# Performance work log

Hardware: AMD Instinct MI355X
Metric: run time of the kernel (lower is better)

Reference implementation:

```python
import jax, jax.numpy as jnp
import numpy as np

H = 128      # hidden_dim
ED = 16      # edge_dim
N = 50000    # n_nodes
E = 500000   # n_edges
B = 1
EPS = 1e-5


def setup_inputs() -> dict:
    key = jax.random.key(0)
    ks = jax.random.split(key, 16)
    s = 0.02
    inp = {
        "h": jax.random.normal(ks[0], (B, N, H), jnp.float32),
        "edge_attr": jax.random.normal(ks[1], (B, E, ED), jnp.float32),
        "edge_index": jax.random.randint(ks[2], (E, 2), 0, N, jnp.int32),
        # src_proj
        "src_W": jax.random.normal(ks[3], (H, H), jnp.float32) * s,
        "src_b": jnp.zeros((H,), jnp.float32),
        # edge_net: Linear(2H+ED -> H), GELU, Linear(H -> 2H)
        "e1_W": jax.random.normal(ks[4], (2 * H + ED, H), jnp.float32) * s,
        "e1_b": jnp.zeros((H,), jnp.float32),
        "e2_W": jax.random.normal(ks[5], (H, 2 * H), jnp.float32) * s,
        "e2_b": jnp.zeros((2 * H,), jnp.float32),
        # self_proj / agg_proj
        "self_W": jax.random.normal(ks[6], (H, H), jnp.float32) * s,
        "self_b": jnp.zeros((H,), jnp.float32),
        "agg_W": jax.random.normal(ks[7], (H, H), jnp.float32) * s,
        "agg_b": jnp.zeros((H,), jnp.float32),
        # LayerNorm
        "ln_g": jnp.ones((H,), jnp.float32),
        "ln_b": jnp.zeros((H,), jnp.float32),
    }
    return inp


def reference(h, edge_attr, edge_index, src_W, src_b, e1_W, e1_b, e2_W, e2_b,
              self_W, self_b, agg_W, agg_b, ln_g, ln_b):
    src = edge_index[:, 0]
    dst = edge_index[:, 1]

    h_src = h[:, src, :]                      # [B, E, H]
    h_dst = h[:, dst, :]                      # [B, E, H]
    edge_input = jnp.concatenate([h_src, h_dst, edge_attr], axis=-1)  # [B, E, 2H+ED]

    hid = jax.nn.gelu(edge_input @ e1_W + e1_b, approximate=False)    # [B, E, H]
    edge_ctx = hid @ e2_W + e2_b                                      # [B, E, 2H]
    gate, shift = jnp.split(edge_ctx, 2, axis=-1)
    msg = jax.nn.sigmoid(gate) * (h_src @ src_W + src_b) + shift      # [B, E, H]

    # scatter-add over destination nodes
    agg = jnp.zeros_like(h).at[:, dst, :].add(msg)                    # [B, N, H]
    indeg = jnp.maximum(jnp.zeros((N,), h.dtype).at[dst].add(1.0), 1.0)
    agg = agg / indeg[None, :, None]

    update = (h @ self_W + self_b) + (agg @ agg_W + agg_b)
    x = h + jax.nn.gelu(update, approximate=False)

    mu = jnp.mean(x, axis=-1, keepdims=True)
    var = jnp.var(x, axis=-1, keepdims=True)
    return (x - mu) / jnp.sqrt(var + EPS) * ln_g + ln_b
```

## Files before the change

### kernel.cpp

```cpp
#include <hip/hip_runtime.h>
#include <hip/hip_bf16.h>
#include <math.h>

#define NN 50000
#define NE 500000
#define LN_EPS 1e-5f

typedef __attribute__((ext_vector_type(8))) short short8;
typedef __attribute__((ext_vector_type(4))) float f32x4;

__device__ __forceinline__ unsigned short f2bf(float f) {
    unsigned int u = __float_as_uint(f);
    u = (u + 0x7FFFu + ((u >> 16) & 1u)) >> 16;
    return (unsigned short)u;
}
__device__ __forceinline__ float bf2f(unsigned short b) {
    return __uint_as_float(((unsigned int)b) << 16);
}
__device__ __forceinline__ float sigm_f(float x) {
    return 1.0f / (1.0f + __expf(-x));
}
__device__ __forceinline__ float gelu_fast(float x) {
    return x * sigm_f(1.5957691f * fmaf(0.044715f * x * x, x, x));
}

__global__ __launch_bounds__(256) void pack_kernel(
    const float* __restrict__ src_W, const float* __restrict__ e1_W,
    const float* __restrict__ e2_W,
    const float* __restrict__ self_W, const float* __restrict__ agg_W,
    unsigned short* __restrict__ p1, unsigned short* __restrict__ p2,
    unsigned short* __restrict__ p3, float2* __restrict__ p4)
{
    const int fid = blockIdx.x * 256 + threadIdx.x;
    if (fid < 6144) {
        const int g = fid / 384, t = fid % 384;
        const int nn = g >> 2, kk = g & 3;
        const int w = t / 64, lane = t & 63, lo = lane & 15, hi = lane >> 4;
        const int c = w * 64 + nn * 16 + lo;
        short8 v;
        #pragma unroll
        for (int j = 0; j < 8; ++j) {
            const int k = kk * 32 + hi * 8 + j;
            float wv;
            if (c < 128)      wv = src_W[k * 128 + c];
            else if (c < 256) wv = e1_W[k * 128 + (c - 128)];
            else              wv = e1_W[(128 + k) * 128 + (c - 256)];
            v[j] = (short)f2bf(wv);
        }
        *(short8*)(p1 + (g * 384 + t) * 8) = v;
    } else if (fid < 10240) {
        const int f = fid - 6144;
        const int g = f / 256, t = f % 256;
        const int nn = g >> 3, kk = g & 7;
        const int w = t / 64, lane = t & 63, lo = lane & 15, hi = lane >> 4;
        const int c = w * 32 + nn * 16 + lo;
        short8 v;
        #pragma unroll
        for (int j = 0; j < 8; ++j) {
            const int k = kk * 32 + hi * 8 + j;
            const float wv = (k < 128) ? self_W[k * 128 + c] : agg_W[(k - 128) * 128 + c];
            v[j] = (short)f2bf(wv);
        }
        *(short8*)(p2 + (g * 256 + t) * 8) = v;
    } else if (fid < 14336) {
        const int f = fid - 10240;
        const int g = f / 256, t = f % 256;
        const int nn = g >> 2, kk = g & 3;
        const int w = t / 64, lane = t & 63, lo = lane & 15, hi = lane >> 4;
        const int nbase = (nn < 2) ? (w * 32 + nn * 16) : (128 + w * 32 + (nn - 2) * 16);
        const int n = nbase + lo;
        short8 v;
        #pragma unroll
        for (int j = 0; j < 8; ++j) {
            const int k = kk * 32 + hi * 8 + j;
            v[j] = (short)f2bf(e2_W[k * 256 + n]);
        }
        *(short8*)(p3 + (g * 256 + t) * 8) = v;
    } else if (fid < 15360) {
        const int f = fid - 14336;
        const int lane = f / 16, k = f % 16;
        p4[lane * 16 + k] = make_float2(e1_W[(256 + k) * 128 + 2 * lane],
                                        e1_W[(256 + k) * 128 + 2 * lane + 1]);
    }
}

__global__ __launch_bounds__(384) void node_pre_kernel(
    const float* __restrict__ h,
    const float* __restrict__ src_b, const float* __restrict__ e1_b,
    const unsigned short* __restrict__ p1,
    unsigned short* __restrict__ hswb,
    unsigned short* __restrict__ a1b,
    unsigned short* __restrict__ b1b)
{
    const int tid = threadIdx.x;
    const int lane = tid & 63;
    const int w = tid >> 6;
    const int lo = lane & 15, hi = lane >> 4;
    const int m0 = blockIdx.x * 64;

    short8 bf[4][4];
    #pragma unroll
    for (int nn = 0; nn < 4; ++nn)
        #pragma unroll
        for (int kk = 0; kk < 4; ++kk)
            bf[kk][nn] = *(const short8*)(p1 + ((nn * 4 + kk) * 384 + tid) * 8);

    f32x4 acc[4][4];
    #pragma unroll
    for (int mm = 0; mm < 4; ++mm)
        #pragma unroll
        for (int nn = 0; nn < 4; ++nn)
            acc[mm][nn] = (f32x4){0.f, 0.f, 0.f, 0.f};

    #pragma unroll
    for (int mm = 0; mm < 4; ++mm) {
        int row = m0 + mm * 16 + lo;
        if (row >= NN) row = NN - 1;
        short8 af[4];
        #pragma unroll
        for (int kk = 0; kk < 4; ++kk) {
            const float* pp = h + row * 128 + kk * 32 + hi * 8;
            const float4 q0 = *(const float4*)pp;
            const float4 q1 = *(const float4*)(pp + 4);
            short8 v;
            v[0] = (short)f2bf(q0.x); v[1] = (short)f2bf(q0.y);
            v[2] = (short)f2bf(q0.z); v[3] = (short)f2bf(q0.w);
            v[4] = (short)f2bf(q1.x); v[5] = (short)f2bf(q1.y);
            v[6] = (short)f2bf(q1.z); v[7] = (short)f2bf(q1.w);
            af[kk] = v;
        }
        #pragma unroll
        for (int nn = 0; nn < 4; ++nn)
            #pragma unroll
            for (int kk = 0; kk < 4; ++kk)
                acc[mm][nn] = __builtin_amdgcn_mfma_f32_16x16x32_bf16(
                    af[kk], bf[kk][nn], acc[mm][nn], 0, 0, 0);
    }

    #pragma unroll
    for (int mm = 0; mm < 4; ++mm) {
        #pragma unroll
        for (int nn = 0; nn < 4; ++nn) {
            const int c = w * 64 + nn * 16 + lo;
            #pragma unroll
            for (int r = 0; r < 4; ++r) {
                const int row = m0 + mm * 16 + hi * 4 + r;
                if (row < NN) {
                    const float v = acc[mm][nn][r];
                    if (c < 128)      hswb[row * 128 + c]       = f2bf(v + src_b[c]);
                    else if (c < 256) a1b [row * 128 + (c-128)] = f2bf(v + e1_b[c-128]);
                    else              b1b [row * 128 + (c-256)] = f2bf(v);
                }
            }
        }
    }
}

__global__ __launch_bounds__(256) void hist_kernel(
    const int* __restrict__ edge_index, int* __restrict__ deg)
{
    const int e = blockIdx.x * 256 + threadIdx.x;
    if (e < NE) atomicAdd(&deg[edge_index[2 * e + 1]], 1);
}

__global__ __launch_bounds__(1024) void scan_kernel(
    const int* __restrict__ deg, int* __restrict__ cursor)
{
    __shared__ int sums[1024];
    const int t = threadIdx.x;
    const int chunk = (NN + 1023) / 1024;
    const int i0 = t * chunk;
    int s = 0;
    for (int i = 0; i < chunk; ++i) {
        const int idx = i0 + i;
        if (idx < NN) s += deg[idx];
    }
    sums[t] = s;
    __syncthreads();
    for (int off = 1; off < 1024; off <<= 1) {
        const int v = (t >= off) ? sums[t - off] : 0;
        __syncthreads();
        sums[t] += v;
        __syncthreads();
    }
    int run = (t > 0) ? sums[t - 1] : 0;
    for (int i = 0; i < chunk; ++i) {
        const int idx = i0 + i;
        if (idx < NN) {
            cursor[idx] = run;
            run += deg[idx];
        }
    }
}

__global__ __launch_bounds__(256) void scatter_kernel(
    const int* __restrict__ edge_index, const float* __restrict__ edge_attr,
    int* __restrict__ cursor,
    int* __restrict__ s_sorted, int* __restrict__ d_sorted,
    unsigned short* __restrict__ ea_sorted)
{
    const int e = blockIdx.x * 256 + threadIdx.x;
    if (e < NE) {
        const int s = edge_index[2 * e];
        const int d = edge_index[2 * e + 1];
        const int pos = atomicAdd(&cursor[d], 1);
        s_sorted[pos] = s;
        d_sorted[pos] = d;
        const float4 q0 = *(const float4*)(edge_attr + e * 16);
        const float4 q1 = *(const float4*)(edge_attr + e * 16 + 4);
        const float4 q2 = *(const float4*)(edge_attr + e * 16 + 8);
        const float4 q3 = *(const float4*)(edge_attr + e * 16 + 12);
        short8 vl, vh;
        vl[0] = (short)f2bf(q0.x); vl[1] = (short)f2bf(q0.y);
        vl[2] = (short)f2bf(q0.z); vl[3] = (short)f2bf(q0.w);
        vl[4] = (short)f2bf(q1.x); vl[5] = (short)f2bf(q1.y);
        vl[6] = (short)f2bf(q1.z); vl[7] = (short)f2bf(q1.w);
        vh[0] = (short)f2bf(q2.x); vh[1] = (short)f2bf(q2.y);
        vh[2] = (short)f2bf(q2.z); vh[3] = (short)f2bf(q2.w);
        vh[4] = (short)f2bf(q3.x); vh[5] = (short)f2bf(q3.y);
        vh[6] = (short)f2bf(q3.z); vh[7] = (short)f2bf(q3.w);
        *(short8*)(ea_sorted + (size_t)pos * 16)     = vl;
        *(short8*)(ea_sorted + (size_t)pos * 16 + 8) = vh;
    }
}

__global__ __launch_bounds__(256, 2) void edge_kernel(
    const unsigned short* __restrict__ ea_sorted,
    const int* __restrict__ s_sorted, const int* __restrict__ d_sorted,
    const unsigned short* __restrict__ p3, const float2* __restrict__ p4,
    const float* __restrict__ e2_b,
    const unsigned short* __restrict__ hswb,
    const unsigned short* __restrict__ a1b, const unsigned short* __restrict__ b1b,
    float* __restrict__ agg, int nblocks)
{
    __shared__ unsigned int hid32[64 * 64];
    __shared__ unsigned int hswt[64 * 64];
    __shared__ int s_lds[2][64];
    __shared__ int d_lds[2][64];

    const int tid = threadIdx.x;
    const int lane = tid & 63;
    const int w = __builtin_amdgcn_readfirstlane(tid >> 6);
    const int lo = lane & 15, hi = lane >> 4;

    float2 e1c[16];
    #pragma unroll
    for (int k = 0; k < 16; ++k) e1c[k] = p4[lane * 16 + k];

    short8 bf[4][4];
    #pragma unroll
    for (int nn = 0; nn < 4; ++nn)
        #pragma unroll
        for (int kk = 0; kk < 4; ++kk)
            bf[kk][nn] = *(const short8*)(p3 + ((nn * 4 + kk) * 256 + tid) * 8);
    float bg[2], bs[2];
    #pragma unroll
    for (int nn = 0; nn < 2; ++nn) {
        bg[nn] = e2_b[w * 32 + nn * 16 + lo];
        bs[nn] = e2_b[128 + w * 32 + nn * 16 + lo];
    }

    const int chunk = (nblocks + (int)gridDim.x - 1) / (int)gridDim.x;
    const int t0 = blockIdx.x * chunk;
    const int t1 = min(t0 + chunk, nblocks);
    if (t0 >= t1) return;

    if (tid < 64) {
        const int ti = t0 * 64 + tid;
        s_lds[0][tid] = (ti < NE) ? s_sorted[ti] : 0;
        d_lds[0][tid] = (ti < NE) ? d_sorted[ti] : -1;
    }
    __syncthreads();

    int p = 0;
    for (int t = t0; t < t1; ++t) {
        const long base = (long)t * 64;

        #pragma unroll
        for (int half = 0; half < 2; ++half) {
            unsigned int av[8], bv[8], hv[8];
            #pragma unroll
            for (int u = 0; u < 8; ++u) {
                const int er = w * 16 + half * 8 + u;
                const int s = s_lds[p][er];
                int d = d_lds[p][er]; if (d < 0) d = 0;
                av[u] = *(const unsigned int*)(a1b  + (size_t)s * 128 + 2 * lane);
                bv[u] = *(const unsigned int*)(b1b  + (size_t)d * 128 + 2 * lane);
                hv[u] = *(const unsigned int*)(hswb + (size_t)s * 128 + 2 * lane);
            }
            #pragma unroll
            for (int u = 0; u < 8; ++u) {
                const int er = w * 16 + half * 8 + u;
                hswt[er * 64 + (lane ^ (((er >> 2) & 3) << 3))] = hv[u];
                float tA = bf2f((unsigned short)(av[u] & 0xFFFFu))
                         + bf2f((unsigned short)(bv[u] & 0xFFFFu));
                float tB = bf2f((unsigned short)(av[u] >> 16))
                         + bf2f((unsigned short)(bv[u] >> 16));
                const short8 eaL = *(const short8*)(ea_sorted + (base + er) * 16);
                const short8 eaH = *(const short8*)(ea_sorted + (base + er) * 16 + 8);
                #pragma unroll
                for (int k = 0; k < 8; ++k) {
                    const float e = bf2f((unsigned short)eaL[k]);
                    tA = fmaf(e, e1c[k].x, tA);
                    tB = fmaf(e, e1c[k].y, tB);
                }
                #pragma unroll
                for (int k = 0; k < 8; ++k) {
                    const float e = bf2f((unsigned short)eaH[k]);
                    tA = fmaf(e, e1c[8 + k].x, tA);
                    tB = fmaf(e, e1c[8 + k].y, tB);
                }
                tA = gelu_fast(tA);
                tB = gelu_fast(tB);
                const unsigned int hp = (unsigned int)f2bf(tA) | ((unsigned int)f2bf(tB) << 16);
                const int ch = (lane >> 2) ^ (er & 7);
                hid32[er * 64 + ch * 4 + (lane & 3)] = hp;
            }
        }

        int sN = 0, dN = -1;
        const bool more = (t + 1 < t1);
        if (more && tid < 64) {
            const int ti = (t + 1) * 64 + tid;
            if (ti < NE) { sN = s_sorted[ti]; dN = d_sorted[ti]; }
        }
        __syncthreads();

        f32x4 acc[4][4];
        #pragma unroll
        for (int mm = 0; mm < 4; ++mm)
            #pragma unroll
            for (int nn = 0; nn < 4; ++nn)
                acc[mm][nn] = (f32x4){0.f, 0.f, 0.f, 0.f};

        #pragma unroll
        for (int mm = 0; mm < 4; ++mm) {
            const int row = mm * 16 + lo;
            short8 af[4];
            #pragma unroll
            for (int kk = 0; kk < 4; ++kk) {
                const int sb = ((kk * 4 + hi) ^ (row & 7)) << 4;
                af[kk] = *(const short8*)((const char*)hid32 + row * 256 + sb);
            }
            #pragma unroll
            for (int nn = 0; nn < 4; ++nn)
                #pragma unroll
                for (int kk = 0; kk < 4; ++kk)
                    acc[mm][nn] = __builtin_amdgcn_mfma_f32_16x16x32_bf16(
                        af[kk], bf[kk][nn], acc[mm][nn], 0, 0, 0);
        }

        #pragma unroll
        for (int mm = 0; mm < 4; ++mm) {
            #pragma unroll
            for (int nn = 0; nn < 2; ++nn) {
                const int c = w * 32 + nn * 16 + lo;
                int pd = -1;
                float pend = 0.f;
                #pragma unroll
                for (int r = 0; r < 4; ++r) {
                    const int er = mm * 16 + hi * 4 + r;
                    const int d = d_lds[p][er];
                    if (d >= 0) {
                        const float g  = acc[mm][nn][r]     + bg[nn];
                        const float sh = acc[mm][nn + 2][r] + bs[nn];
                        const unsigned int hw =
                            hswt[er * 64 + ((c >> 1) ^ (((er >> 2) & 3) << 3))];
                        const float hval =
                            bf2f((unsigned short)((c & 1) ? (hw >> 16) : (hw & 0xFFFFu)));
                        const float msg = sigm_f(g) * hval + sh;
                        if (d != pd) {
                            if (pd >= 0) unsafeAtomicAdd(&agg[(size_t)pd * 128 + c], pend);
                            pd = d; pend = 0.f;
                        }
                        pend += msg;
                    }
                }
                if (pd >= 0) unsafeAtomicAdd(&agg[(size_t)pd * 128 + c], pend);
            }
        }

        if (more && tid < 64) {
            s_lds[p ^ 1][tid] = sN;
            d_lds[p ^ 1][tid] = dN;
        }
        __syncthreads();
        p ^= 1;
    }
}

__global__ __launch_bounds__(256) void node_post_kernel(
    const float* __restrict__ h,
    const float* __restrict__ self_b, const float* __restrict__ agg_b,
    const float* __restrict__ ln_g, const float* __restrict__ ln_b,
    const float* __restrict__ agg, const int* __restrict__ deg,
    const unsigned short* __restrict__ p2,
    float* __restrict__ out)
{
    __shared__ float x_lds[64 * 129];
    const int tid = threadIdx.x;
    const int lane = tid & 63;
    const int w = tid >> 6;
    const int lo = lane & 15, hi = lane >> 4;
    const int m0 = blockIdx.x * 64;

    short8 bf[8][2];
    #pragma unroll
    for (int nn = 0; nn < 2; ++nn)
        #pragma unroll
        for (int kk = 0; kk < 8; ++kk)
            bf[kk][nn] = *(const short8*)(p2 + ((nn * 8 + kk) * 256 + tid) * 8);

    f32x4 acc[4][2];
    #pragma unroll
    for (int mm = 0; mm < 4; ++mm)
        #pragma unroll
        for (int nn = 0; nn < 2; ++nn)
            acc[mm][nn] = (f32x4){0.f, 0.f, 0.f, 0.f};

    #pragma unroll
    for (int mm = 0; mm < 4; ++mm) {
        int row = m0 + mm * 16 + lo;
        if (row >= NN) row = NN - 1;
        const float rdeg = 1.0f / fmaxf((float)deg[row], 1.0f);
        short8 af[8];
        #pragma unroll
        for (int kk = 0; kk < 4; ++kk) {
            const float* pp = h + row * 128 + kk * 32 + hi * 8;
            const float4 q0 = *(const float4*)pp;
            const float4 q1 = *(const float4*)(pp + 4);
            short8 v;
            v[0] = (short)f2bf(q0.x); v[1] = (short)f2bf(q0.y);
            v[2] = (short)f2bf(q0.z); v[3] = (short)f2bf(q0.w);
            v[4] = (short)f2bf(q1.x); v[5] = (short)f2bf(q1.y);
            v[6] = (short)f2bf(q1.z); v[7] = (short)f2bf(q1.w);
            af[kk] = v;
        }
        #pragma unroll
        for (int kk = 4; kk < 8; ++kk) {
            const float* pp = agg + row * 128 + (kk - 4) * 32 + hi * 8;
            const float4 q0 = *(const float4*)pp;
            const float4 q1 = *(const float4*)(pp + 4);
            short8 v;
            v[0] = (short)f2bf(q0.x * rdeg); v[1] = (short)f2bf(q0.y * rdeg);
            v[2] = (short)f2bf(q0.z * rdeg); v[3] = (short)f2bf(q0.w * rdeg);
            v[4] = (short)f2bf(q1.x * rdeg); v[5] = (short)f2bf(q1.y * rdeg);
            v[6] = (short)f2bf(q1.z * rdeg); v[7] = (short)f2bf(q1.w * rdeg);
            af[kk] = v;
        }
        #pragma unroll
        for (int nn = 0; nn < 2; ++nn)
            #pragma unroll
            for (int kk = 0; kk < 8; ++kk)
                acc[mm][nn] = __builtin_amdgcn_mfma_f32_16x16x32_bf16(
                    af[kk], bf[kk][nn], acc[mm][nn], 0, 0, 0);
    }

    #pragma unroll
    for (int mm = 0; mm < 4; ++mm) {
        #pragma unroll
        for (int nn = 0; nn < 2; ++nn) {
            const int c = w * 32 + nn * 16 + lo;
            const float bsum = self_b[c] + agg_b[c];
            #pragma unroll
            for (int r = 0; r < 4; ++r) {
                const int rl = mm * 16 + hi * 4 + r;
                int row = m0 + rl;
                if (row >= NN) row = NN - 1;
                const float upd = acc[mm][nn][r] + bsum;
                x_lds[rl * 129 + c] = h[row * 128 + c] + gelu_fast(upd);
            }
        }
    }
    __syncthreads();

    const int rrow = tid >> 2;
    const int part = tid & 3;
    float sum = 0.f, ss = 0.f;
    #pragma unroll
    for (int i = 0; i < 32; ++i) {
        const float v = x_lds[rrow * 129 + part * 32 + i];
        sum += v; ss += v * v;
    }
    sum += __shfl_xor(sum, 1); ss += __shfl_xor(ss, 1);
    sum += __shfl_xor(sum, 2); ss += __shfl_xor(ss, 2);
    const float mu = sum * (1.0f / 128.0f);
    const float var = ss * (1.0f / 128.0f) - mu * mu;
    const float rstd = rsqrtf(var + LN_EPS);
    const int grow = m0 + rrow;
    if (grow < NN) {
        #pragma unroll
        for (int i = 0; i < 32; ++i) {
            const int c = part * 32 + i;
            const float v = x_lds[rrow * 129 + c];
            out[grow * 128 + c] = (v - mu) * rstd * ln_g[c] + ln_b[c];
        }
    }
}

extern "C" void kernel_launch(void* const* d_in, const int* in_sizes, int n_in,
                              void* d_out, int out_size, void* d_ws, size_t ws_size,
                              hipStream_t stream) {
    const float* h         = (const float*)d_in[0];
    const float* edge_attr = (const float*)d_in[1];
    const int*   edge_index= (const int*)  d_in[2];
    const float* src_W     = (const float*)d_in[3];
    const float* src_b     = (const float*)d_in[4];
    const float* e1_W      = (const float*)d_in[5];
    const float* e1_b      = (const float*)d_in[6];
    const float* e2_W      = (const float*)d_in[7];
    const float* e2_b      = (const float*)d_in[8];
    const float* self_W    = (const float*)d_in[9];
    const float* self_b    = (const float*)d_in[10];
    const float* agg_W     = (const float*)d_in[11];
    const float* agg_b     = (const float*)d_in[12];
    const float* ln_g      = (const float*)d_in[13];
    const float* ln_b      = (const float*)d_in[14];
    float* out = (float*)d_out;

    char* ws = (char*)d_ws;
    unsigned short* hswb = (unsigned short*)(ws);
    unsigned short* a1b  = (unsigned short*)(ws + 12800000);
    unsigned short* b1b  = (unsigned short*)(ws + 25600000);
    float* agg         = (float*)(ws + 38400000);
    int*   deg         = (int*)  (ws + 64000000);
    int*   cursor      = (int*)  (ws + 64200000);
    int*   s_sorted    = (int*)  (ws + 64400000);
    int*   d_sorted    = (int*)  (ws + 66400000);
    unsigned short* p1 = (unsigned short*)(ws + 68400000);
    unsigned short* p2 = (unsigned short*)(ws + 68500000);
    unsigned short* p3 = (unsigned short*)(ws + 68600000);
    float2*         p4 = (float2*)        (ws + 68700000);
    unsigned short* ea_sorted = (unsigned short*)(ws + 68710000);

    hipMemsetAsync(agg, 0, 25600000 + 200000, stream);

    pack_kernel<<<60, 256, 0, stream>>>(src_W, e1_W, e2_W, self_W, agg_W,
                                        p1, p2, p3, p4);

    hist_kernel<<<(NE + 255) / 256, 256, 0, stream>>>(edge_index, deg);
    scan_kernel<<<1, 1024, 0, stream>>>(deg, cursor);
    scatter_kernel<<<(NE + 255) / 256, 256, 0, stream>>>(
        edge_index, edge_attr, cursor, s_sorted, d_sorted, ea_sorted);

    node_pre_kernel<<<(NN + 63) / 64, 384, 0, stream>>>(
        h, src_b, e1_b, p1, hswb, a1b, b1b);

    const int nblocks = (NE + 63) / 64;
    edge_kernel<<<512, 256, 0, stream>>>(
        ea_sorted, s_sorted, d_sorted, p3, p4, e2_b,
        hswb, a1b, b1b, agg, nblocks);

    node_post_kernel<<<(NN + 63) / 64, 256, 0, stream>>>(
        h, self_b, agg_b, ln_g, ln_b, agg, deg, p2, out);
}
```

Baseline: 614.4 us.

## Parallelize degree scan across blocks and split edge MFMA epilogue to raise occupancy

Replaces the single-block 1024-thread serial-chunk prefix scan with a two-kernel multi-block scan: per-block partial sums first, then a per-block offset plus local scan. The edge kernel's MFMA accumulator array is split into two column-pair passes, which lowers live accumulator registers, and launch bounds and grid size go from 2 to 3 blocks per CU. The aim is to remove a serial scan bottleneck and hide gather latency with more occupancy. In exchange, the hid tile fragments are reloaded from LDS twice and there is one extra kernel launch.

New measurement: 812.9 us. 1.32x slower.

```diff
diff --git a/kernel.cpp b/kernel.cpp
--- a/kernel.cpp
+++ b/kernel.cpp
@@ -4,6 +4,7 @@
 
 #define NN 50000
 #define NE 500000
+#define NB 196
 #define LN_EPS 1e-5f
 
 typedef __attribute__((ext_vector_type(8))) short short8;
@@ -163,34 +164,49 @@
     if (e < NE) atomicAdd(&deg[edge_index[2 * e + 1]], 1);
 }
 
-__global__ __launch_bounds__(1024) void scan_kernel(
-    const int* __restrict__ deg, int* __restrict__ cursor)
-{
-    __shared__ int sums[1024];
+__global__ __launch_bounds__(256) void scan1_kernel(
+    const int* __restrict__ deg, int* __restrict__ partial)
+{
+    __shared__ int red[256];
     const int t = threadIdx.x;
-    const int chunk = (NN + 1023) / 1024;
-    const int i0 = t * chunk;
-    int s = 0;
-    for (int i = 0; i < chunk; ++i) {
-        const int idx = i0 + i;
-        if (idx < NN) s += deg[idx];
-    }
-    sums[t] = s;
+    const int idx = blockIdx.x * 256 + t;
+    red[t] = (idx < NN) ? deg[idx] : 0;
     __syncthreads();
-    for (int off = 1; off < 1024; off <<= 1) {
-        const int v = (t >= off) ? sums[t - off] : 0;
+    #pragma unroll
+    for (int o = 128; o > 0; o >>= 1) {
+        if (t < o) red[t] += red[t + o];
         __syncthreads();
-        sums[t] += v;
+    }
+    if (t == 0) partial[blockIdx.x] = red[0];
+}
+
+__global__ __launch_bounds__(256) void scan2_kernel(
+    const int* __restrict__ deg, const int* __restrict__ partial,
+    int* __restrict__ cursor)
+{
+    __shared__ int sp[256];
+    __shared__ int ls[256];
+    const int t = threadIdx.x;
+    sp[t] = (t < NB && t < (int)blockIdx.x) ? partial[t] : 0;
+    __syncthreads();
+    #pragma unroll
+    for (int o = 128; o > 0; o >>= 1) {
+        if (t < o) sp[t] += sp[t + o];
         __syncthreads();
     }
-    int run = (t > 0) ? sums[t - 1] : 0;
-    for (int i = 0; i < chunk; ++i) {
-        const int idx = i0 + i;
-        if (idx < NN) {
-            cursor[idx] = run;
-            run += deg[idx];
-        }
-    }
+    const int base = sp[0];
+    const int idx = blockIdx.x * 256 + t;
+    const int v = (idx < NN) ? deg[idx] : 0;
+    ls[t] = v;
+    __syncthreads();
+    #pragma unroll
+    for (int o = 1; o < 256; o <<= 1) {
+        const int x = (t >= o) ? ls[t - o] : 0;
+        __syncthreads();
+        ls[t] += x;
+        __syncthreads();
+    }
+    if (idx < NN) cursor[idx] = base + ls[t] - v;
 }
 
 __global__ __launch_bounds__(256) void scatter_kernel(
@@ -224,7 +240,7 @@
     }
 }
 
-__global__ __launch_bounds__(256, 2) void edge_kernel(
+__global__ __launch_bounds__(256, 3) void edge_kernel(
     const unsigned short* __restrict__ ea_sorted,
     const int* __restrict__ s_sorted, const int* __restrict__ d_sorted,
     const unsigned short* __restrict__ p3, const float2* __restrict__ p4,
@@ -274,7 +290,6 @@
 
     int p = 0;
     for (int t = t0; t < t1; ++t) {
-        const long base = (long)t * 64;
 
         #pragma unroll
         for (int half = 0; half < 2; ++half) {
@@ -288,6 +303,7 @@
                 bv[u] = *(const unsigned int*)(b1b  + (size_t)d * 128 + 2 * lane);
                 hv[u] = *(const unsigned int*)(hswb + (size_t)s * 128 + 2 * lane);
             }
+            const long base = (long)t * 64;
             #pragma unroll
             for (int u = 0; u < 8; ++u) {
                 const int er = w * 16 + half * 8 + u;
@@ -326,44 +342,43 @@
         }
         __syncthreads();
 
-        f32x4 acc[4][4];
-        #pragma unroll
-        for (int mm = 0; mm < 4; ++mm)
-            #pragma unroll
-            for (int nn = 0; nn < 4; ++nn)
-                acc[mm][nn] = (f32x4){0.f, 0.f, 0.f, 0.f};
-
-        #pragma unroll
-        for (int mm = 0; mm < 4; ++mm) {
-            const int row = mm * 16 + lo;
-            short8 af[4];
-            #pragma unroll
-            for (int kk = 0; kk < 4; ++kk) {
-                const int sb = ((kk * 4 + hi) ^ (row & 7)) << 4;
-                af[kk] = *(const short8*)((const char*)hid32 + row * 256 + sb);
-            }
-            #pragma unroll
-            for (int nn = 0; nn < 4; ++nn)
+        #pragma unroll
+        for (int np = 0; np < 2; ++np) {
+            f32x4 accg[4], accs[4];
+            #pragma unroll
+            for (int mm = 0; mm < 4; ++mm) {
+                accg[mm] = (f32x4){0.f, 0.f, 0.f, 0.f};
+                accs[mm] = (f32x4){0.f, 0.f, 0.f, 0.f};
+            }
+            #pragma unroll
+            for (int mm = 0; mm < 4; ++mm) {
+                const int row = mm * 16 + lo;
+                short8 af[4];
                 #pragma unroll
-                for (int kk = 0; kk < 4; ++kk)
-                    acc[mm][nn] = __builtin_amdgcn_mfma_f32_16x16x32_bf16(
-                        af[kk], bf[kk][nn], acc[mm][nn], 0, 0, 0);
-        }
-
-        #pragma unroll
-        for (int mm = 0; mm < 4; ++mm) {
-            #pragma unroll
-            for (int nn = 0; nn < 2; ++nn) {
-                const int c = w * 32 + nn * 16 + lo;
-                int pd = -1;
-                float pend = 0.f;
+                for (int kk = 0; kk < 4; ++kk) {
+                    const int sb = ((kk * 4 + hi) ^ (row & 7)) << 4;
+                    af[kk] = *(const short8*)((const char*)hid32 + row * 256 + sb);
+                }
+                #pragma unroll
+                for (int kk = 0; kk < 4; ++kk) {
+                    accg[mm] = __builtin_amdgcn_mfma_f32_16x16x32_bf16(
+                        af[kk], bf[kk][np],     accg[mm], 0, 0, 0);
+                    accs[mm] = __builtin_amdgcn_mfma_f32_16x16x32_bf16(
+                        af[kk], bf[kk][np + 2], accs[mm], 0, 0, 0);
+                }
+            }
+            const int c = w * 32 + np * 16 + lo;
+            int pd = -1;
+            float pend = 0.f;
+            #pragma unroll
+            for (int mm = 0; mm < 4; ++mm) {
                 #pragma unroll
                 for (int r = 0; r < 4; ++r) {
                     const int er = mm * 16 + hi * 4 + r;
                     const int d = d_lds[p][er];
                     if (d >= 0) {
-                        const float g  = acc[mm][nn][r]     + bg[nn];
-                        const float sh = acc[mm][nn + 2][r] + bs[nn];
+                        const float g  = accg[mm][r] + bg[np];
+                        const float sh = accs[mm][r] + bs[np];
                         const unsigned int hw =
                             hswt[er * 64 + ((c >> 1) ^ (((er >> 2) & 3) << 3))];
                         const float hval =
@@ -376,8 +391,8 @@
                         pend += msg;
                     }
                 }
-                if (pd >= 0) unsafeAtomicAdd(&agg[(size_t)pd * 128 + c], pend);
-            }
+            }
+            if (pd >= 0) unsafeAtomicAdd(&agg[(size_t)pd * 128 + c], pend);
         }
 
         if (more && tid < 64) {
@@ -531,6 +546,7 @@
     unsigned short* p2 = (unsigned short*)(ws + 68500000);
     unsigned short* p3 = (unsigned short*)(ws + 68600000);
     float2*         p4 = (float2*)        (ws + 68700000);
+    int*   partial     = (int*)  (ws + 68708192);
     unsigned short* ea_sorted = (unsigned short*)(ws + 68710000);
 
     hipMemsetAsync(agg, 0, 25600000 + 200000, stream);
@@ -539,7 +555,8 @@
                                         p1, p2, p3, p4);
 
     hist_kernel<<<(NE + 255) / 256, 256, 0, stream>>>(edge_index, deg);
-    scan_kernel<<<1, 1024, 0, stream>>>(deg, cursor);
+    scan1_kernel<<<NB, 256, 0, stream>>>(deg, partial);
+    scan2_kernel<<<NB, 256, 0, stream>>>(deg, partial, cursor);
     scatter_kernel<<<(NE + 255) / 256, 256, 0, stream>>>(
         edge_index, edge_attr, cursor, s_sorted, d_sorted, ea_sorted);
 
@@ -547,7 +564,7 @@
         h, src_b, e1_b, p1, hswb, a1b, b1b);
 
     const int nblocks = (NE + 63) / 64;
-    edge_kernel<<<512, 256, 0, stream>>>(
+    edge_kernel<<<768, 256, 0, stream>>>(
         ea_sorted, s_sorted, d_sorted, p3, p4, e2_b,
         hswb, a1b, b1b, agg, nblocks);
 
```
